# Kernel optimization log

Hardware: AMD Instinct MI355X
Metric: run time of the kernel (lower is better)

The kernel has to match this reference:

```python
import jax, jax.numpy as jnp
import numpy as np

# Static conv hyperparameters (match init_kwargs)
STRIDE = (1, 1)
PAD = (1, 1)
DIL = (1, 1)
GROUPS = 1
DG = 1  # num_deformable_groups


def setup_inputs() -> dict:
    key = jax.random.key(0)
    k1, k2, k3 = jax.random.split(key, 3)
    B, C, H, W = 4, 256, 64, 64
    OC, kh, kw = 256, 3, 3
    x = jax.random.normal(k1, (B, C, H, W), dtype=jnp.float32)
    # offset: [B, DG*2*kh*kw, Ho, Wo], ordered (tap, [dy, dx]) per deformable group
    offset = jax.random.normal(k2, (B, DG * 2 * kh * kw, H, W), dtype=jnp.float32)
    n = C * kh * kw
    stdv = 1.0 / np.sqrt(n)
    weight = jax.random.uniform(k3, (OC, C // GROUPS, kh, kw), dtype=jnp.float32,
                                minval=-stdv, maxval=stdv)
    return {"x": x, "offset": offset, "weight": weight}


def _deform_conv(x, offset, weight):
    B, C, H, W = x.shape
    OC, Cg_w, kh, kw = weight.shape
    sh, sw = STRIDE
    ph, pw = PAD
    dh, dw = DIL
    Ho = (H + 2 * ph - (dh * (kh - 1) + 1)) // sh + 1
    Wo = (W + 2 * pw - (dw * (kw - 1) + 1)) // sw + 1
    K = kh * kw
    Cg = C // DG  # channels per deformable group

    # offsets: [B, DG, K, 2, Ho, Wo]; channel 0 = dy (h), channel 1 = dx (w)
    off = offset.reshape(B, DG, K, 2, Ho, Wo)

    # base (undeformed) sampling positions per tap
    ki, kj = jnp.meshgrid(jnp.arange(kh), jnp.arange(kw), indexing='ij')
    base_h = (jnp.arange(Ho) * sh - ph)[None, :] + (ki.reshape(-1) * dh)[:, None]  # [K, Ho]
    base_w = (jnp.arange(Wo) * sw - pw)[None, :] + (kj.reshape(-1) * dw)[:, None]  # [K, Wo]

    pos_h = base_h[None, None, :, :, None].astype(x.dtype) + off[:, :, :, 0]  # [B,DG,K,Ho,Wo]
    pos_w = base_w[None, None, :, None, :].astype(x.dtype) + off[:, :, :, 1]  # [B,DG,K,Ho,Wo]

    h0f = jnp.floor(pos_h)
    w0f = jnp.floor(pos_w)
    lh = pos_h - h0f  # fractional parts
    lw = pos_w - w0f
    h0 = h0f.astype(jnp.int32)
    w0 = w0f.astype(jnp.int32)

    xg = x.reshape(B, DG, Cg, H * W)

    def gather(hi, wi):
        # zero-padded gather: out-of-range corners contribute 0 (mmcv DCNv1 semantics)
        valid = (hi >= 0) & (hi < H) & (wi >= 0) & (wi < W)  # [B,DG,K,Ho,Wo]
        idx = jnp.clip(hi, 0, H - 1) * W + jnp.clip(wi, 0, W - 1)
        flat = idx.reshape(B, DG, 1, K * Ho * Wo)
        vals = jnp.take_along_axis(
            xg, jnp.broadcast_to(flat, (B, DG, Cg, K * Ho * Wo)), axis=3)
        vals = vals.reshape(B, DG, Cg, K, Ho, Wo)
        return vals * valid[:, :, None].astype(x.dtype)

    # bilinear interpolation over 4 corners -> im2col columns [B,DG,Cg,K,Ho,Wo]
    cols = (gather(h0, w0) * ((1 - lh) * (1 - lw))[:, :, None]
            + gather(h0, w0 + 1) * ((1 - lh) * lw)[:, :, None]
            + gather(h0 + 1, w0) * (lh * (1 - lw))[:, :, None]
            + gather(h0 + 1, w0 + 1) * (lh * lw)[:, :, None])

    # grouped GEMM: columns x weight
    cols = cols.reshape(B, GROUPS, C // GROUPS, K, Ho, Wo)
    wg = weight.reshape(GROUPS, OC // GROUPS, Cg_w, K)
    out = jnp.einsum('gock,bgckhw->bgohw', wg, cols)
    return out.reshape(B, OC, Ho, Wo)


def reference(x, offset, weight):
    return _deform_conv(x, offset, weight)
```

## Files before the change

### kernel.cpp

```cpp
#include <hip/hip_runtime.h>
#include <hip/hip_bf16.h>
#include <math.h>


constexpr int B  = 4;
constexpr int C  = 256;
constexpr int H  = 64;
constexpr int W  = 64;
constexpr int OC = 256;
constexpr int Ho = 64;
constexpr int Wo = 64;

constexpr int NT     = 64;
constexpr int CHUNKS = 72;
constexpr int WROW   = 40;

constexpr size_t WB_ELTS  = (size_t)CHUNKS * 16 * 512;
constexpr size_t XB_ELTS  = (size_t)B * 8 * 4096 * 32;
constexpr size_t OUT_ELTS = (size_t)B * OC * Ho * Wo;

typedef __attribute__((ext_vector_type(8))) short bf16x8;
typedef __attribute__((ext_vector_type(4))) float f32x4;

__device__ __forceinline__ float bf_lo(unsigned u) {
    union { unsigned i; float f; } c; c.i = u << 16; return c.f;
}
__device__ __forceinline__ float bf_hi(unsigned u) {
    union { unsigned i; float f; } c; c.i = u & 0xffff0000u; return c.f;
}
__device__ __forceinline__ ushort fbf(float f) {
    __hip_bfloat16 h = __float2bfloat16(f); return *(ushort*)&h;
}

__global__ __launch_bounds__(256)
void prep_all(const float* __restrict__ x, const float* __restrict__ wt,
              ushort* __restrict__ xb, ushort* __restrict__ wB)
{
    __shared__ ushort sx[128 * WROW];
    __shared__ ushort sw[CHUNKS * WROW];
    const int t = threadIdx.x;

    if (blockIdx.x < 1024) {
        const int blk = blockIdx.x;
        const int hwb = blk & 31;
        const int cb  = (blk >> 5) & 7;
        const int b   = blk >> 8;
        const int hw0 = hwb << 7;
        const int lhw = t & 127, chalf = t >> 7;
        #pragma unroll
        for (int i = 0; i < 16; ++i) {
            const int c = i * 2 + chalf;
            sx[lhw * WROW + c] =
                fbf(x[(((size_t)(b * 256 + cb * 32 + c)) << 12) + hw0 + lhw]);
        }
        __syncthreads();
        const int whw = t >> 1, wh = t & 1;
        const uint4 v0 = *(const uint4*)&sx[whw * WROW + wh * 16];
        const uint4 v1 = *(const uint4*)&sx[whw * WROW + wh * 16 + 8];
        uint4* dst = (uint4*)(xb + ((size_t)((b * 8 + cb) * 4096 + hw0) << 5));
        dst[whw * 4 + wh * 2 + 0] = v0;
        dst[whw * 4 + wh * 2 + 1] = v1;
    } else {
        const int oc = blockIdx.x - 1024;
        const int c  = t, chb = c >> 5, kk = c & 31;
        const float* wp = wt + ((size_t)oc * C + c) * 9;
        #pragma unroll
        for (int tap = 0; tap < 9; ++tap)
            sw[(tap * 8 + chb) * WROW + kk] = fbf(wp[tap]);
        __syncthreads();
        const int og = oc >> 4, mr = oc & 15;
        for (int i = t; i < CHUNKS * 4; i += 256) {
            const int ch = i >> 2, kq = i & 3;
            *(uint4*)(wB + ((size_t)ch * 16 + og) * 512 + (kq * 16 + mr) * 8) =
                *(const uint4*)&sw[ch * WROW + kq * 8];
        }
    }
}

struct GathRegs { uint4 c00, c01, c10, c11; float4 mw; };

__global__ __launch_bounds__(512, 4)
void dcn_mfma(const ushort* __restrict__ xb, const float* __restrict__ off,
              const ushort* __restrict__ wB, float* __restrict__ po)
{
    __shared__ __align__(16) ushort s_col[2][2][NT * WROW];
    __shared__ __align__(16) float4 s_mw[9 * NT];
    __shared__ __align__(8)  int2   s_midx[9 * NT];

    const int xcd = blockIdx.x & 7;
    const int ii  = blockIdx.x >> 3;
    const int b   = xcd & 3;
    const int khalf = ii & 1;
    const int ho  = ((xcd >> 2) << 5) + (ii >> 1);
    const int ch0 = khalf * 36;
    float* outp = po + (size_t)khalf * OUT_ELTS;
    const int tid = threadIdx.x;

    for (int s = tid; s < 9 * NT; s += 512) {
        const int n   = s & 63;
        const int tap = s >> 6;
        const float dy = off[((size_t)(b * 18 + 2 * tap)     * Ho + ho) * Wo + n];
        const float dx = off[((size_t)(b * 18 + 2 * tap + 1) * Ho + ho) * Wo + n];
        const float ph = (float)(ho - 1 + tap / 3) + dy;
        const float pw = (float)(n  - 1 + tap % 3) + dx;
        const float h0f = floorf(ph), w0f = floorf(pw);
        const int h0 = (int)h0f, w0 = (int)w0f;
        const float lh = ph - h0f, lw = pw - w0f;
        const int wb = min(max(w0, 0), W - 2);
        const int ht = min(max(h0, 0), H - 1);
        const int hb = min(max(h0 + 1, 0), H - 1);
        const float s0 = (wb == w0) ? (1.f - lw) : ((wb == w0 + 1) ? lw : 0.f);
        const float s1 = (wb + 1 == w0 + 1) ? lw : ((wb + 1 == w0) ? (1.f - lw) : 0.f);
        const float wtp = (h0 >= 0 && h0 < H)         ? (1.f - lh) : 0.f;
        const float wbt = (h0 + 1 >= 0 && h0 + 1 < H) ? lh         : 0.f;
        s_midx[s] = make_int2(ht * W + wb, hb * W + wb);
        s_mw[s]   = make_float4(wtp * s0, wtp * s1, wbt * s0, wbt * s1);
    }

    const int lane = tid & 63;
    const int wv   = tid >> 6;
    const int kq   = lane >> 4;
    const int mr   = lane & 15;

    const int kc_t = tid >> 8;
    const int st   = tid & 255;
    const int sn   = st >> 2;
    const int sgg  = st & 3;
    const ushort* xb_sg = xb + ((size_t)b << 20) + (sgg << 3);

    f32x4 acc[2][4];
    #pragma unroll
    for (int mt = 0; mt < 2; ++mt)
        #pragma unroll
        for (int nt = 0; nt < 4; ++nt)
            acc[mt][nt] = (f32x4){0.f, 0.f, 0.f, 0.f};

    auto issueg = [&](int p, GathRegs& g) {
        const int ch  = ch0 + 2 * p + kc_t;
        const int tap = ch >> 3;
        const int cb  = ch & 7;
        const int2 mi = s_midx[tap * NT + sn];
        g.mw = s_mw[tap * NT + sn];
        const ushort* xp = xb_sg + ((size_t)cb << 17);
        g.c00 = *(const uint4*)(xp + ((size_t)mi.x << 5));
        g.c01 = *(const uint4*)(xp + (((size_t)mi.x + 1) << 5));
        g.c10 = *(const uint4*)(xp + ((size_t)mi.y << 5));
        g.c11 = *(const uint4*)(xp + (((size_t)mi.y + 1) << 5));
    };
    auto sampfma = [&](const GathRegs& g, int buf) {
        union { ushort pk[8]; uint4 v; } u;
        const unsigned a00[4] = {g.c00.x, g.c00.y, g.c00.z, g.c00.w};
        const unsigned a01[4] = {g.c01.x, g.c01.y, g.c01.z, g.c01.w};
        const unsigned a10[4] = {g.c10.x, g.c10.y, g.c10.z, g.c10.w};
        const unsigned a11[4] = {g.c11.x, g.c11.y, g.c11.z, g.c11.w};
        #pragma unroll
        for (int j = 0; j < 4; ++j) {
            const float vlo = g.mw.x * bf_lo(a00[j]) + g.mw.y * bf_lo(a01[j])
                            + g.mw.z * bf_lo(a10[j]) + g.mw.w * bf_lo(a11[j]);
            const float vhi = g.mw.x * bf_hi(a00[j]) + g.mw.y * bf_hi(a01[j])
                            + g.mw.z * bf_hi(a10[j]) + g.mw.w * bf_hi(a11[j]);
            u.pk[2 * j]     = fbf(vlo);
            u.pk[2 * j + 1] = fbf(vhi);
        }
        *(uint4*)&s_col[buf][kc_t][sn * WROW + sgg * 8] = u.v;
    };
    auto phase = [&](int p, const GathRegs& gcur, int buf) {
        sampfma(gcur, buf);
        bf16x8 wf[2][2];
        const int chb = ch0 + 2 * p;
        #pragma unroll
        for (int kc = 0; kc < 2; ++kc)
            #pragma unroll
            for (int mt = 0; mt < 2; ++mt)
                wf[kc][mt] = *(const bf16x8*)
                    (wB + ((size_t)(chb + kc) * 16 + wv * 2 + mt) * 512 + lane * 8);
        asm volatile("s_waitcnt lgkmcnt(0)" ::: "memory");
        __builtin_amdgcn_s_barrier();
        __builtin_amdgcn_sched_barrier(0);
        __builtin_amdgcn_s_setprio(1);
        #pragma unroll
        for (int kc = 0; kc < 2; ++kc)
            #pragma unroll
            for (int nt = 0; nt < 4; ++nt) {
                const bf16x8 bfr = *(const bf16x8*)
                    &s_col[buf][kc][(nt * 16 + mr) * WROW + kq * 8];
                #pragma unroll
                for (int mt = 0; mt < 2; ++mt)
                    acc[mt][nt] = __builtin_amdgcn_mfma_f32_16x16x32_bf16(
                        wf[kc][mt], bfr, acc[mt][nt], 0, 0, 0);
            }
        __builtin_amdgcn_s_setprio(0);
    };

    __syncthreads();

    GathRegs gA, gB;
    issueg(0, gA);

    #pragma unroll 1
    for (int it = 0; it < 9; ++it) {
        issueg(2 * it + 1, gB);
        phase(2 * it, gA, 0);
        if (it < 8) issueg(2 * it + 2, gA);
        phase(2 * it + 1, gB, 1);
    }

    #pragma unroll
    for (int mt = 0; mt < 2; ++mt)
        #pragma unroll
        for (int nt = 0; nt < 4; ++nt)
            #pragma unroll
            for (int r = 0; r < 4; ++r) {
                const int oc = wv * 32 + mt * 16 + kq * 4 + r;
                const int wo = nt * 16 + mr;
                outp[((size_t)(b * OC + oc) * Ho + ho) * Wo + wo] = acc[mt][nt][r];
            }
}

__global__ __launch_bounds__(256)
void reduce2(const float4* __restrict__ p0, const float4* __restrict__ p1,
             float4* __restrict__ out)
{
    const int i = blockIdx.x * 256 + threadIdx.x;
    const float4 a = p0[i], b = p1[i];
    out[i] = make_float4(a.x + b.x, a.y + b.y, a.z + b.z, a.w + b.w);
}

extern "C" void kernel_launch(void* const* d_in, const int* in_sizes, int n_in,
                              void* d_out, int out_size, void* d_ws, size_t ws_size,
                              hipStream_t stream)
{
    const float* x   = (const float*)d_in[0];
    const float* off = (const float*)d_in[1];
    const float* wt  = (const float*)d_in[2];
    float* out = (float*)d_out;

    ushort* wB = (ushort*)d_ws;
    ushort* xb = wB + WB_ELTS;
    float*  po = (float*)(xb + XB_ELTS);

    prep_all<<<1280, 256, 0, stream>>>(x, wt, xb, wB);
    dcn_mfma<<<512, 512, 0, stream>>>(xb, off, wB, po);
    reduce2<<<(int)(OUT_ELTS / 4 / 256), 256, 0, stream>>>(
        (const float4*)po, (const float4*)(po + OUT_ELTS), (float4*)out);
}
```

Measured before the change: 113.6 us.

## Merge K-split into one 1024-thread block with in-LDS reduction

The K dimension was previously split across two blocks that wrote two partial output buffers, followed by a separate reduce kernel. Now one block of 1024 threads (16 waves) handles both K halves: waves 8-15 take the second channel pair of each step, and the two halves are summed through LDS before coalesced float4 stores to the final output. This removes the partial-buffer traffic and the extra kernel launch. The cost is half as many blocks (256), larger blocks with more barriers, and a serialized reduction epilogue.

```diff
diff --git a/kernel.cpp b/kernel.cpp
--- a/kernel.cpp
+++ b/kernel.cpp
@@ -14,10 +14,11 @@
 constexpr int NT     = 64;
 constexpr int CHUNKS = 72;
 constexpr int WROW   = 40;
+constexpr int XROW   = 40;
+constexpr int RSTR   = 68;
 
 constexpr size_t WB_ELTS  = (size_t)CHUNKS * 16 * 512;
 constexpr size_t XB_ELTS  = (size_t)B * 8 * 4096 * 32;
-constexpr size_t OUT_ELTS = (size_t)B * OC * Ho * Wo;
 
 typedef __attribute__((ext_vector_type(8))) short bf16x8;
 typedef __attribute__((ext_vector_type(4))) float f32x4;
@@ -36,8 +37,8 @@
 void prep_all(const float* __restrict__ x, const float* __restrict__ wt,
               ushort* __restrict__ xb, ushort* __restrict__ wB)
 {
-    __shared__ ushort sx[128 * WROW];
-    __shared__ ushort sw[CHUNKS * WROW];
+    __shared__ ushort sx[128 * XROW];
+    __shared__ ushort sw[CHUNKS * XROW];
     const int t = threadIdx.x;
 
     if (blockIdx.x < 1024) {
@@ -50,13 +51,13 @@
         #pragma unroll
         for (int i = 0; i < 16; ++i) {
             const int c = i * 2 + chalf;
-            sx[lhw * WROW + c] =
+            sx[lhw * XROW + c] =
                 fbf(x[(((size_t)(b * 256 + cb * 32 + c)) << 12) + hw0 + lhw]);
         }
         __syncthreads();
         const int whw = t >> 1, wh = t & 1;
-        const uint4 v0 = *(const uint4*)&sx[whw * WROW + wh * 16];
-        const uint4 v1 = *(const uint4*)&sx[whw * WROW + wh * 16 + 8];
+        const uint4 v0 = *(const uint4*)&sx[whw * XROW + wh * 16];
+        const uint4 v1 = *(const uint4*)&sx[whw * XROW + wh * 16 + 8];
         uint4* dst = (uint4*)(xb + ((size_t)((b * 8 + cb) * 4096 + hw0) << 5));
         dst[whw * 4 + wh * 2 + 0] = v0;
         dst[whw * 4 + wh * 2 + 1] = v1;
@@ -66,39 +67,35 @@
         const float* wp = wt + ((size_t)oc * C + c) * 9;
         #pragma unroll
         for (int tap = 0; tap < 9; ++tap)
-            sw[(tap * 8 + chb) * WROW + kk] = fbf(wp[tap]);
+            sw[(tap * 8 + chb) * XROW + kk] = fbf(wp[tap]);
         __syncthreads();
         const int og = oc >> 4, mr = oc & 15;
         for (int i = t; i < CHUNKS * 4; i += 256) {
             const int ch = i >> 2, kq = i & 3;
             *(uint4*)(wB + ((size_t)ch * 16 + og) * 512 + (kq * 16 + mr) * 8) =
-                *(const uint4*)&sw[ch * WROW + kq * 8];
+                *(const uint4*)&sw[ch * XROW + kq * 8];
         }
     }
 }
 
 struct GathRegs { uint4 c00, c01, c10, c11; float4 mw; };
 
-__global__ __launch_bounds__(512, 4)
+__global__ __launch_bounds__(1024, 4)
 void dcn_mfma(const ushort* __restrict__ xb, const float* __restrict__ off,
-              const ushort* __restrict__ wB, float* __restrict__ po)
+              const ushort* __restrict__ wB, float* __restrict__ out)
 {
-    __shared__ __align__(16) ushort s_col[2][2][NT * WROW];
+    __shared__ __align__(16) ushort s_col[2][4][NT * WROW];
     __shared__ __align__(16) float4 s_mw[9 * NT];
     __shared__ __align__(8)  int2   s_midx[9 * NT];
 
     const int xcd = blockIdx.x & 7;
-    const int ii  = blockIdx.x >> 3;
     const int b   = xcd & 3;
-    const int khalf = ii & 1;
-    const int ho  = ((xcd >> 2) << 5) + (ii >> 1);
-    const int ch0 = khalf * 36;
-    float* outp = po + (size_t)khalf * OUT_ELTS;
+    const int ho  = ((xcd >> 2) << 5) + (blockIdx.x >> 3);
     const int tid = threadIdx.x;
 
-    for (int s = tid; s < 9 * NT; s += 512) {
-        const int n   = s & 63;
-        const int tap = s >> 6;
+    if (tid < 9 * NT) {
+        const int n   = tid & 63;
+        const int tap = tid >> 6;
         const float dy = off[((size_t)(b * 18 + 2 * tap)     * Ho + ho) * Wo + n];
         const float dx = off[((size_t)(b * 18 + 2 * tap + 1) * Ho + ho) * Wo + n];
         const float ph = (float)(ho - 1 + tap / 3) + dy;
@@ -113,12 +110,14 @@
         const float s1 = (wb + 1 == w0 + 1) ? lw : ((wb + 1 == w0) ? (1.f - lw) : 0.f);
         const float wtp = (h0 >= 0 && h0 < H)         ? (1.f - lh) : 0.f;
         const float wbt = (h0 + 1 >= 0 && h0 + 1 < H) ? lh         : 0.f;
-        s_midx[s] = make_int2(ht * W + wb, hb * W + wb);
-        s_mw[s]   = make_float4(wtp * s0, wtp * s1, wbt * s0, wbt * s1);
+        s_midx[tid] = make_int2(ht * W + wb, hb * W + wb);
+        s_mw[tid]   = make_float4(wtp * s0, wtp * s1, wbt * s0, wbt * s1);
     }
 
     const int lane = tid & 63;
     const int wv   = tid >> 6;
+    const int ocg  = wv & 7;
+    const int kside= wv >> 3;
     const int kq   = lane >> 4;
     const int mr   = lane & 15;
 
@@ -136,7 +135,7 @@
             acc[mt][nt] = (f32x4){0.f, 0.f, 0.f, 0.f};
 
     auto issueg = [&](int p, GathRegs& g) {
-        const int ch  = ch0 + 2 * p + kc_t;
+        const int ch  = 4 * p + kc_t;
         const int tap = ch >> 3;
         const int cb  = ch & 7;
         const int2 mi = s_midx[tap * NT + sn];
@@ -167,13 +166,13 @@
     auto phase = [&](int p, const GathRegs& gcur, int buf) {
         sampfma(gcur, buf);
         bf16x8 wf[2][2];
-        const int chb = ch0 + 2 * p;
+        const int chb = 4 * p + 2 * kside;
         #pragma unroll
         for (int kc = 0; kc < 2; ++kc)
             #pragma unroll
             for (int mt = 0; mt < 2; ++mt)
                 wf[kc][mt] = *(const bf16x8*)
-                    (wB + ((size_t)(chb + kc) * 16 + wv * 2 + mt) * 512 + lane * 8);
+                    (wB + ((size_t)(chb + kc) * 16 + ocg * 2 + mt) * 512 + lane * 8);
         asm volatile("s_waitcnt lgkmcnt(0)" ::: "memory");
         __builtin_amdgcn_s_barrier();
         __builtin_amdgcn_sched_barrier(0);
@@ -183,7 +182,7 @@
             #pragma unroll
             for (int nt = 0; nt < 4; ++nt) {
                 const bf16x8 bfr = *(const bf16x8*)
-                    &s_col[buf][kc][(nt * 16 + mr) * WROW + kq * 8];
+                    &s_col[buf][2 * kside + kc][(nt * 16 + mr) * WROW + kq * 8];
                 #pragma unroll
                 for (int mt = 0; mt < 2; ++mt)
                     acc[mt][nt] = __builtin_amdgcn_mfma_f32_16x16x32_bf16(
@@ -205,25 +204,38 @@
         phase(2 * it + 1, gB, 1);
     }
 
-    #pragma unroll
-    for (int mt = 0; mt < 2; ++mt)
-        #pragma unroll
-        for (int nt = 0; nt < 4; ++nt)
-            #pragma unroll
-            for (int r = 0; r < 4; ++r) {
-                const int oc = wv * 32 + mt * 16 + kq * 4 + r;
-                const int wo = nt * 16 + mr;
-                outp[((size_t)(b * OC + oc) * Ho + ho) * Wo + wo] = acc[mt][nt][r];
-            }
-}
-
-__global__ __launch_bounds__(256)
-void reduce2(const float4* __restrict__ p0, const float4* __restrict__ p1,
-             float4* __restrict__ out)
-{
-    const int i = blockIdx.x * 256 + threadIdx.x;
-    const float4 a = p0[i], b = p1[i];
-    out[i] = make_float4(a.x + b.x, a.y + b.y, a.z + b.z, a.w + b.w);
+    float* red = (float*)s_col;
+    #pragma unroll 1
+    for (int mt = 0; mt < 2; ++mt) {
+        __syncthreads();
+        if (kside == 1) {
+            #pragma unroll
+            for (int nt = 0; nt < 4; ++nt)
+                #pragma unroll
+                for (int r = 0; r < 4; ++r)
+                    red[(ocg * 16 + kq * 4 + r) * RSTR + nt * 16 + mr] =
+                        acc[mt][nt][r];
+        }
+        __syncthreads();
+        if (kside == 0) {
+            #pragma unroll
+            for (int nt = 0; nt < 4; ++nt)
+                #pragma unroll
+                for (int r = 0; r < 4; ++r) {
+                    const int a = (ocg * 16 + kq * 4 + r) * RSTR + nt * 16 + mr;
+                    red[a] += acc[mt][nt][r];
+                }
+        }
+        __syncthreads();
+        #pragma unroll
+        for (int j = 0; j < 2; ++j) {
+            const int fidx = (wv * 64 + lane) * 2 + j;
+            const int rr = fidx >> 4, q = fidx & 15;
+            const float4 v = *(const float4*)&red[rr * RSTR + q * 4];
+            const int oc = (rr >> 4) * 32 + mt * 16 + (rr & 15);
+            *(float4*)&out[(((size_t)(b * OC + oc) * Ho + ho) << 6) + q * 4] = v;
+        }
+    }
 }
 
 extern "C" void kernel_launch(void* const* d_in, const int* in_sizes, int n_in,
@@ -237,10 +249,7 @@
 
     ushort* wB = (ushort*)d_ws;
     ushort* xb = wB + WB_ELTS;
-    float*  po = (float*)(xb + XB_ELTS);
 
     prep_all<<<1280, 256, 0, stream>>>(x, wt, xb, wB);
-    dcn_mfma<<<512, 512, 0, stream>>>(xb, off, wB, po);
-    reduce2<<<(int)(OUT_ELTS / 4 / 256), 256, 0, stream>>>(
-        (const float4*)po, (const float4*)(po + OUT_ELTS), (float4*)out);
-}
+    dcn_mfma<<<256, 1024, 0, stream>>>(xb, off, wB, out);
+}
```

New measurement: 121.8 us. 7.3% more time.
